# Performance work log

Hardware: AMD Instinct MI355X
Metric: run time of the kernel (lower is better)

The kernel has to match this reference:

```python
import jax, jax.numpy as jnp
import numpy as np


def setup_inputs() -> dict:
    B, L, D, M, S = 4, 1024, 1024, 16, 8
    key = jax.random.key(0)
    ks = jax.random.split(key, 12)
    sd = 0.02
    inp = {
        "hid": jax.random.normal(ks[0], (B, L, D), jnp.float32),
        "src_hid": jax.random.normal(ks[1], (B, L, D), jnp.float32),
        "sp_width": jax.random.randint(ks[2], (B, L), 0, 9),
        "max_sp_len": S,
        "attention_mask": jnp.ones((B, L), bool),
        "src_mask": jnp.ones((B, L), bool),
        # span-start attention (1 head): query/key linears + relative-key embedding table
        "wq_st": sd * jax.random.normal(ks[3], (D, D), jnp.float32),
        "bq_st": jnp.zeros((D,), jnp.float32),
        "wk_st": sd * jax.random.normal(ks[4], (D, D), jnp.float32),
        "bk_st": jnp.zeros((D,), jnp.float32),
        "rel_st": sd * jax.random.normal(ks[5], (2 * M + 1, D), jnp.float32),
        # span-end attention
        "wq_ed": sd * jax.random.normal(ks[6], (D, D), jnp.float32),
        "bq_ed": jnp.zeros((D,), jnp.float32),
        "wk_ed": sd * jax.random.normal(ks[7], (D, D), jnp.float32),
        "bk_ed": jnp.zeros((D,), jnp.float32),
        "rel_ed": sd * jax.random.normal(ks[8], (2 * M + 1, D), jnp.float32),
        # sp_emb: Linear(2D -> D), stored as [2D, D] (x @ W + b)
        "sp_w": sd * jax.random.normal(ks[9], (2 * D, D), jnp.float32),
        "sp_b": jnp.zeros((D,), jnp.float32),
    }
    return inp


def reference(hid, src_hid, sp_width, max_sp_len, attention_mask, src_mask,
              wq_st, bq_st, wk_st, bk_st, rel_st,
              wq_ed, bq_ed, wk_ed, bk_ed, rel_ed, sp_w, sp_b):
    B, L, D = hid.shape
    scale = 1.0 / jnp.sqrt(jnp.float32(D))
    M = (rel_st.shape[0] - 1) // 2
    pos = jnp.arange(L)
    rel_idx = jnp.clip(pos[None, :] - pos[:, None], -M, M) + M          # [L,L]
    rel_idx_b = jnp.broadcast_to(rel_idx[None], (B, L, L))

    amask = (src_mask[:, :, None] & attention_mask[:, None, :]).astype(jnp.float32)  # [B,Lq,Lk]
    attn_w0 = amask / jnp.clip(jnp.sum(amask, 2, keepdims=True), 1e-6)

    def attn(query, wq, bq, wk, bk, rel_tab, mask):
        # single-head relative-position attention; returns attention weights [B,L,L]
        q = (query @ wq + bq) * scale                                   # [B,L,D]
        k = hid @ wk + bk                                               # [B,L,D]
        sc = jnp.einsum('bqd,bkd->bqk', q, k)
        # q . rel_emb[rel_idx[q_pos,k_pos]]: contract with table then gather (avoids [L,L,D])
        rel_sc = jnp.take_along_axis(jnp.einsum('bqd,rd->bqr', q, rel_tab), rel_idx_b, axis=2)
        sc = jnp.where(mask > 0, sc + rel_sc, -1e18)
        return jax.nn.softmax(sc, axis=-1)

    def upd(attn_w, hidp):
        # weighted sum of hid + linear + relu (dropout is identity in eval)
        hidc = jnp.einsum('bqk,bkd->bqd', attn_w, hid)
        return jax.nn.relu(jnp.concatenate([hidp, hidc], axis=2) @ sp_w + sp_b)

    sts, eds, masks = [attn_w0], [attn_w0], []
    hid1, hid2 = src_hid, src_hid
    for i in range(max_sp_len):
        m = (i < sp_width).astype(jnp.float32)                          # [B,L]
        masks.append(m)
        mask_i = m[:, :, None] * amask                                  # [B,L,L]
        hid1 = upd(sts[-1], hid1)
        sts.append(attn(hid1, wq_st, bq_st, wk_st, bk_st, rel_st, mask_i))
        hid2 = upd(eds[-1], hid2)
        eds.append(attn(hid2, wq_ed, bq_ed, wk_ed, bk_ed, rel_ed, mask_i))

    return (jnp.stack(sts[1:], -2),   # [B,L,S,L]
            jnp.stack(eds[1:], -2),   # [B,L,S,L]
            jnp.stack(masks, -1))     # [B,L,S]
```

## Files before the change

kernel.cpp:

```cpp
#include <hip/hip_runtime.h>

typedef unsigned short u16;
typedef __attribute__((ext_vector_type(8))) short bh8;
typedef __attribute__((ext_vector_type(4))) float f4;

__device__ __forceinline__ u16 f2b(float x){
  union { float f; unsigned u; } c; c.f = x;
  unsigned r = (c.u + 0x7FFFu + ((c.u >> 16) & 1u)) >> 16;
  return (u16)r;
}
__device__ __forceinline__ float b2f(u16 h){
  union { unsigned u; float f; } c; c.u = ((unsigned)h) << 16; return c.f;
}
__device__ __forceinline__ void gload16(const void* g, void* l){
  __builtin_amdgcn_global_load_lds((const __attribute__((address_space(1))) void*)g,
                                   (__attribute__((address_space(3))) void*)l, 16, 0, 0);
}


__global__ __launch_bounds__(256) void convall_k(const float* __restrict__ hid,
                                                 const float* __restrict__ wq0, const float* __restrict__ wq1,
                                                 const float* __restrict__ wk0, const float* __restrict__ wk1,
                                                 const float* __restrict__ rel0, const float* __restrict__ rel1,
                                                 u16* __restrict__ hidB, u16* __restrict__ wqB,
                                                 u16* __restrict__ wkB, u16* __restrict__ relB){
  long g = (long)blockIdx.x*256 + threadIdx.x;
  if (g >= 2114048L) return;
  const float* src; u16* dst; long off;
  if      (g < 1048576L){ src = hid;  dst = hidB;           off = g; }
  else if (g < 1310720L){ src = wq0;  dst = wqB;            off = g - 1048576L; }
  else if (g < 1572864L){ src = wq1;  dst = wqB + 1048576;  off = g - 1310720L; }
  else if (g < 1835008L){ src = wk0;  dst = wkB;            off = g - 1572864L; }
  else if (g < 2097152L){ src = wk1;  dst = wkB + 1048576;  off = g - 1835008L; }
  else if (g < 2105600L){ src = rel0; dst = relB;           off = g - 2097152L; }
  else                  { src = rel1; dst = relB + 131072;  off = g - 2105600L; }
  f4 v = *(const f4*)(src + off*4);
  ushort4 pk = make_ushort4(f2b(v[0]), f2b(v[1]), f2b(v[2]), f2b(v[3]));
  *(ushort4*)(dst + off*4) = pk;
}

__global__ __launch_bounds__(256) void uniform0_k(const int* __restrict__ spw, float* __restrict__ out){
  int bl = blockIdx.x;
  if (spw[bl] != 0) return;
  f4 t = {0.0009765625f, 0.0009765625f, 0.0009765625f, 0.0009765625f};
  float* b0 = out + (size_t)bl*8192;
  float* b1 = out + 33554432ull + (size_t)bl*8192;
  #pragma unroll
  for (int i = 0; i < 8; i++){
    ((f4*)(b0 + (size_t)i*1024))[threadIdx.x] = t;
    ((f4*)(b1 + (size_t)i*1024))[threadIdx.x] = t;
  }
}

__global__ __launch_bounds__(256) void trans_k(const float* __restrict__ in, u16* __restrict__ out,
                                               int R, int C){
  __shared__ u16 t[32][33];
  int bx = blockIdx.x*32, by = blockIdx.y*32;
  int tx = threadIdx.x & 31, ty = threadIdx.x >> 5;
  #pragma unroll
  for (int j = 0; j < 32; j += 8) t[ty+j][tx] = f2b(in[(size_t)(by+ty+j)*C + bx+tx]);
  __syncthreads();
  #pragma unroll
  for (int j = 0; j < 32; j += 8) out[(size_t)(bx+ty+j)*R + by+tx] = t[tx][ty+j];
}

__global__ __launch_bounds__(256) void sort_k(const int* __restrict__ spw, int* __restrict__ perm,
                                              int* __restrict__ cnt, float* __restrict__ mout){
  int b = blockIdx.x, t = threadIdx.x;
  __shared__ int hist[9], start[9];
  if (t < 9) hist[t] = 0;
  __syncthreads();
  for (int l = t; l < 1024; l += 256) atomicAdd(&hist[spw[b*1024 + l]], 1);
  __syncthreads();
  if (t == 0){
    int acc = 0;
    for (int w = 8; w >= 0; w--){ start[w] = acc; acc += hist[w]; }
  }
  __syncthreads();
  if (t < 8) cnt[b*8 + t] = start[t];
  __syncthreads();
  for (int l = t; l < 1024; l += 256){
    int w = spw[b*1024 + l];
    float* mo = mout + ((size_t)b*1024 + l)*8;
    #pragma unroll
    for (int i = 0; i < 8; i++) mo[i] = (i < w) ? 1.0f : 0.0f;
    int pos = atomicAdd(&start[w], 1);
    perm[b*1024 + pos] = l;
  }
}

__global__ __launch_bounds__(256) void gather_k(const float* __restrict__ srch, const int* __restrict__ perm,
                                                u16* __restrict__ hb){
  int blk = blockIdx.x;
  int z = blk >> 10, c = blk & 1023;
  int ro = perm[z*1024 + c];
  const float* src = srch + ((size_t)z*1024 + ro)*1024;
  u16* dst = hb + ((size_t)z*1024 + c)*1024;
  for (int d = threadIdx.x; d < 1024; d += 256) dst[d] = f2b(src[d]);
}

__global__ __launch_bounds__(256) void dots_k(const float* __restrict__ wq0, const float* __restrict__ wq1,
                                              const float* __restrict__ wk0, const float* __restrict__ wk1,
                                              const float* __restrict__ bq0, const float* __restrict__ bq1,
                                              const float* __restrict__ bk0, const float* __restrict__ bk1,
                                              const float* __restrict__ rel0, const float* __restrict__ rel1,
                                              float* __restrict__ ubuf, float* __restrict__ c0buf,
                                              float* __restrict__ bqbk, float* __restrict__ cba){
  int row = blockIdx.x*4 + (threadIdx.x >> 6);
  int lane = threadIdx.x & 63;
  if (row >= 4164) return;
  const float *a, *v;
  int kind = 0, oi = 0, br_s = 0, br_r = 0;
  if      (row < 1024){ a = wk0 + (size_t)row*1024; v = bq0; oi = row; }
  else if (row < 2048){ a = wk1 + (size_t)(row-1024)*1024; v = bq1; oi = row; }
  else if (row < 3072){ a = wq0 + (size_t)(row-2048)*1024; v = bk0; kind = 1; oi = row-2048; }
  else if (row < 4096){ a = wq1 + (size_t)(row-3072)*1024; v = bk1; kind = 1; oi = row-3072+1024; }
  else if (row < 4162){ int idx = row-4096; br_s = idx/33; br_r = idx%33;
                        a = (br_s ? rel1 : rel0) + (size_t)br_r*1024; v = br_s ? bq1 : bq0; kind = 2; }
  else                { int s2 = row-4162; a = s2 ? bq1 : bq0; v = s2 ? bk1 : bk0; kind = 3; oi = s2; }
  const f4* ap = (const f4*)a;
  const f4* vp = (const f4*)v;
  float acc = 0.0f;
  #pragma unroll
  for (int p = 0; p < 4; p++){
    f4 x = ap[lane + 64*p], y = vp[lane + 64*p];
    acc += x[0]*y[0] + x[1]*y[1] + x[2]*y[2] + x[3]*y[3];
  }
  #pragma unroll
  for (int off = 32; off > 0; off >>= 1) acc += __shfl_xor(acc, off, 64);
  if (lane == 0){
    if (kind == 0) ubuf[oi] = acc;
    else if (kind == 1) c0buf[oi] = acc;
    else if (kind == 2){
      float w = acc*0.03125f;
      for (int b = 0; b < 4; b++) cba[(br_s*4 + b)*1152 + 1024 + br_r] = w;
    } else bqbk[oi] = acc;
  }
}

__global__ __launch_bounds__(256) void cba_k(const float* __restrict__ hid, const float* __restrict__ u,
                                             const float* __restrict__ bqbk, float* __restrict__ cba){
  int row = blockIdx.x*4 + (threadIdx.x >> 6);
  int lane = threadIdx.x & 63;
  int z = row >> 10, l = row & 1023, b = z & 3, s = z >> 2;
  const f4* hp = (const f4*)(hid + ((size_t)b*1024 + l)*1024);
  const f4* up = (const f4*)(u + s*1024);
  float acc = 0.0f;
  #pragma unroll
  for (int p = 0; p < 4; p++){
    f4 a = hp[lane + 64*p], c = up[lane + 64*p];
    acc += a[0]*c[0] + a[1]*c[1] + a[2]*c[2] + a[3]*c[3];
  }
  #pragma unroll
  for (int off = 32; off > 0; off >>= 1) acc += __shfl_xor(acc, off, 64);
  if (!lane) cba[z*1152 + l] = (acc + bqbk[s])*0.03125f;
}

__global__ __launch_bounds__(256) void meanh2_k(const u16* __restrict__ H2T, float* __restrict__ mh){
  int row = blockIdx.x*4 + (threadIdx.x >> 6);
  int lane = threadIdx.x & 63;
  const u16* p = H2T + (size_t)row*1024 + lane*16;
  float s = 0.0f;
  #pragma unroll
  for (int j = 0; j < 16; j++) s += b2f(p[j]);
  #pragma unroll
  for (int off = 32; off > 0; off >>= 1) s += __shfl_xor(s, off, 64);
  if (lane == 0) mh[row] = s * 0.0009765625f;
}

__global__ __launch_bounds__(256) void softmax_k(const u16* __restrict__ scB, float* __restrict__ outF,
                                                 u16* __restrict__ attnP, const float* __restrict__ qrelb,
                                                 const int* __restrict__ cnt, const int* __restrict__ perm,
                                                 const int* __restrict__ spw, int iter){
  int z = blockIdx.x >> 10, c = blockIdx.x & 1023;
  int s = z >> 2, b = z & 3;
  if (c >= cnt[b*8 + iter]) return;
  int ro = perm[b*1024 + c];
  __shared__ float qr[33];
  __shared__ float red[8];
  if (threadIdx.x < 33) qr[threadIdx.x] = qrelb[((size_t)z*1024 + c)*33 + threadIdx.x];
  __syncthreads();
  const u16* sc = scB + ((size_t)z*1024 + c)*1024;
  float* po = outF + (size_t)s*33554432ull + (((size_t)(b*1024 + ro))*8 + (size_t)iter)*1024;
  u16* pr = attnP + ((size_t)z*1024 + c)*1024;
  int t = threadIdx.x;
  float v[4]; float mx = -1e30f;
  #pragma unroll
  for (int j = 0; j < 4; j++){
    int col = t + j*256;
    int d = col - ro; d = d < -16 ? -16 : (d > 16 ? 16 : d);
    v[j] = b2f(sc[col]) + qr[d + 16];
    mx = fmaxf(mx, v[j]);
  }
  #pragma unroll
  for (int off = 32; off > 0; off >>= 1) mx = fmaxf(mx, __shfl_xor(mx, off, 64));
  int wv = t >> 6, ln = t & 63;
  if (ln == 0) red[wv] = mx;
  __syncthreads();
  mx = fmaxf(fmaxf(red[0], red[1]), fmaxf(red[2], red[3]));
  float sm = 0.0f;
  #pragma unroll
  for (int j = 0; j < 4; j++){ v[j] = __expf(v[j] - mx); sm += v[j]; }
  #pragma unroll
  for (int off = 32; off > 0; off >>= 1) sm += __shfl_xor(sm, off, 64);
  if (ln == 0) red[4 + wv] = sm;
  __syncthreads();
  sm = red[4] + red[5] + red[6] + red[7];
  float inv = 1.0f / sm;
  #pragma unroll
  for (int j = 0; j < 4; j++){
    float pv = v[j] * inv;
    po[t + j*256] = pv;
    pr[t + j*256] = f2b(pv);
  }
  int w = spw[b*1024 + ro];
  if (iter == w - 1 && w < 8){
    f4 u = {0.0009765625f, 0.0009765625f, 0.0009765625f, 0.0009765625f};
    for (int j = 1; j <= 7 - iter; j++)
      ((f4*)(po + (size_t)j*1024))[t] = u;
  }
}

template<int MODE>
__global__ __launch_bounds__(256) void gemm_k(
    const u16* __restrict__ A_, const u16* __restrict__ B_,
    const u16* __restrict__ A2_, const u16* __restrict__ B2_,
    const float* __restrict__ e0, const float* __restrict__ e1,
    u16* __restrict__ outB, u16* __restrict__ outB2, float* __restrict__ qrelb,
    const int* __restrict__ cnt, int iter, int azmask)
{
  const int z = blockIdx.z;
  const size_t LD = 1024*1024;
  const int bm = blockIdx.y*128, bn = blockIdx.x*128;
  int s = z >> 2, b = z & 3;
  bool m5h2 = false;
  if constexpr (MODE == 5){ if (z >= 8){ m5h2 = true; b = z - 8; s = 0; } }

  int cntv = 1024;
  if constexpr (MODE == 2 || MODE == 4){
    cntv = cnt[b*8 + iter];
    if (bm >= cntv) return;
  }

  const u16 *A1, *B1, *A2, *B2;
  int lda1 = 1024, ldb1 = 1024, lda2 = 1024, ldb2 = 1024, K = 1024, K1 = 1024;

  if constexpr (MODE == 0){
    if (z < 2){ A1 = A_ + (size_t)z*LD; B1 = B_ + (size_t)z*LD; }
    else {
      if (blockIdx.y > 0) return;
      A1 = A2_ + (size_t)(z-2)*131072;
      B1 = A_ + (size_t)(z-2)*LD;
    }
    A2=A1; B2=B1;
  }
  else if constexpr (MODE == 2){
    A1 = A_ + (size_t)z*LD; B1 = B_ + (size_t)b*LD;
    A2 = A2_ + (size_t)(z & azmask)*LD; B2 = B2_; ldb2 = 2048;
    if (iter == 0){ K = 1024; K1 = 0; } else { K = 2048; K1 = 1024; }
  }
  else if constexpr (MODE == 4){ A1 = A_ + (size_t)(z & azmask)*LD; B1 = B_ + (size_t)z*1179648; A2=A1; B2=B1; }
  else {
    if (!m5h2){ A1 = A_ + (size_t)b*LD; B1 = B_ + (size_t)s*LD; }
    else      { A1 = A2_ + 1024; lda1 = 2048; B1 = B2_ + (size_t)b*LD; }
    A2=A1; B2=B1; lda2=lda1;
  }

  __shared__ __align__(16) u16 lA[16384];
  __shared__ __align__(16) u16 lB[16384];
  const int tid = threadIdx.x, wv = tid >> 6, lane = tid & 63;
  const int wr = (wv >> 1)*64, wc = (wv & 1)*64;
  const int fr = lane & 15, kh = lane >> 4;
  const int stRow = (lane >> 2);
  const int ssw  = ((lane >> 2) & 3) ^ ((lane >> 4) & 3);
  const int stCe = ((lane & 3) ^ ssw)*8;
  const int fsw  = (fr & 3) ^ ((fr >> 2) & 3);
  const int rdSl = (kh ^ fsw)*8;

  auto stage = [&](int bufsel, int k0s){
    const u16 *As, *Bs; int kk, la, lb;
    if (k0s < K1){ As = A1; Bs = B1; kk = k0s; la = lda1; lb = ldb1; }
    else         { As = A2; Bs = B2; kk = k0s - K1; la = lda2; lb = ldb2; }
    #pragma unroll
    for (int c = 0; c < 4; c++){
      const int n = wv*4 + c;
      const int h = n >> 3;
      const int rl = (n & 7)*16 + stRow;
      const int ke = kk + h*32 + stCe;
      gload16(As + (size_t)(bm + rl)*la + ke, (char*)lA + bufsel*16384 + n*1024);
      gload16(Bs + (size_t)(bn + rl)*lb + ke, (char*)lB + bufsel*16384 + n*1024);
    }
  };

  f4 acc[4][4];
  #pragma unroll
  for (int i = 0; i < 4; i++)
    #pragma unroll
    for (int j = 0; j < 4; j++)
      acc[i][j] = f4{0.f, 0.f, 0.f, 0.f};

  stage(0, 0);
  stage(1, 64);

  int cur = 0;
  for (int k0 = 0; k0 < K; k0 += 64){
    if (k0 + 64 < K) asm volatile("s_waitcnt vmcnt(8)" ::: "memory");
    else             asm volatile("s_waitcnt vmcnt(0)" ::: "memory");
    __builtin_amdgcn_s_barrier();
    asm volatile("" ::: "memory");
    const u16* bufA = lA + cur*8192;
    const u16* bufB = lB + cur*8192;
    bh8 af[2][4], bfr[2][4];
    #pragma unroll
    for (int h = 0; h < 2; h++){
      #pragma unroll
      for (int i = 0; i < 4; i++){
        af[h][i]  = *(const bh8*)&bufA[h*4096 + (wr + i*16 + fr)*32 + rdSl];
        bfr[h][i] = *(const bh8*)&bufB[h*4096 + (wc + i*16 + fr)*32 + rdSl];
      }
    }
    if (k0 + 128 < K){
      asm volatile("s_waitcnt lgkmcnt(0)" ::: "memory");
      __builtin_amdgcn_sched_barrier(0);
      __builtin_amdgcn_s_barrier();
      asm volatile("" ::: "memory");
      stage(cur, k0 + 128);
    }
    __builtin_amdgcn_s_setprio(1);
    #pragma unroll
    for (int h = 0; h < 2; h++)
      #pragma unroll
      for (int i = 0; i < 4; i++)
        #pragma unroll
        for (int j = 0; j < 4; j++)
          acc[i][j] = __builtin_amdgcn_mfma_f32_16x16x32_bf16(af[h][i], bfr[h][j], acc[i][j], 0, 0, 0);
    __builtin_amdgcn_s_setprio(0);
    cur ^= 1;
  }

  const int rw = (lane >> 4)*4, cl = lane & 15;
  #pragma unroll
  for (int i = 0; i < 4; i++){
    #pragma unroll
    for (int r = 0; r < 4; r++){
      const int row = bm + wr + i*16 + rw + r;
      if constexpr (MODE == 2 || MODE == 4){ if (row >= cntv) continue; }
      #pragma unroll
      for (int j = 0; j < 4; j++){
        const int col = bn + wc + j*16 + cl;
        float v = acc[i][j][r];
        if constexpr (MODE == 0){
          if (z < 2){
            outB[(size_t)z*LD + (size_t)row*1024 + col] = f2b(v);
          } else if (row < 33){
            u16 vv = f2b(v*0.03125f);
            size_t o = (size_t)(1024 + row)*1024 + col;
            int sx = z - 2;
            #pragma unroll
            for (int bb = 0; bb < 4; bb++)
              outB2[(size_t)(sx*4 + bb)*1179648 + o] = vv;
          }
        } else if constexpr (MODE == 2){
          v += e0[col];
          if (e1) v += e1[b*1024 + col];
          v = fmaxf(v, 0.0f);
          outB[(size_t)z*LD + (size_t)row*1024 + col] = f2b(v);
        } else if constexpr (MODE == 5){
          if (!m5h2)
            outB[(size_t)z*1179648 + (size_t)row*1024 + col] = f2b((v + e0[s*1024 + col])*0.03125f);
          else
            outB2[(size_t)b*LD + (size_t)row*1024 + col] = f2b(v);
        } else {
          v += e0[z*1152 + col];
          if (col < 1024){
            outB[((size_t)z*1024 + row)*1024 + col] = f2b(v);
          } else {
            int rr = col - 1024;
            if (rr < 33) qrelb[((size_t)z*1024 + row)*33 + rr] = v;
          }
        }
      }
    }
  }
}


extern "C" void kernel_launch(void* const* d_in, const int* in_sizes, int n_in,
                              void* d_out, int out_size, void* d_ws, size_t ws_size,
                              hipStream_t stream)
{
  const float* hid    = (const float*)d_in[0];
  const float* srch   = (const float*)d_in[1];
  const int*   spw    = (const int*)d_in[2];
  const float* wq_st  = (const float*)d_in[6];
  const float* bq_st  = (const float*)d_in[7];
  const float* wk_st  = (const float*)d_in[8];
  const float* bk_st  = (const float*)d_in[9];
  const float* rel_st = (const float*)d_in[10];
  const float* wq_ed  = (const float*)d_in[11];
  const float* bq_ed  = (const float*)d_in[12];
  const float* wk_ed  = (const float*)d_in[13];
  const float* bk_ed  = (const float*)d_in[14];
  const float* rel_ed = (const float*)d_in[15];
  const float* sp_w   = (const float*)d_in[16];
  const float* sp_b   = (const float*)d_in[17];
  float* out = (float*)d_out;

  const size_t LD = 1024*1024;
  char* p = (char*)d_ws;
  u16* hidB  = (u16*)p; p += 4*LD*2;
  u16* wqB   = (u16*)p; p += 2*LD*2;
  u16* wkB   = (u16*)p; p += 2*LD*2;
  u16* relB  = (u16*)p; p += 2*131072*2;
  u16* spwT  = (u16*)p; p += 2*LD*2;
  u16* WT    = (u16*)p; p += 2*LD*2;
  u16* H2T   = (u16*)p; p += 4*LD*2;
  u16* Mx    = (u16*)p; p += 8ull*1179648*2;
  u16* attnP = (u16*)p; p += 8*LD*2;
  u16* hbufA = (u16*)p; p += 8*LD*2;
  u16* hbufB = (u16*)p; p += 8*LD*2;
  u16* scB   = (u16*)p; p += 8*LD*2;
  float* qrelb  = (float*)p; p += 8*1024*33*4;
  float* cba    = (float*)p; p += 8*1152*4;
  float* ubuf   = (float*)p; p += 2048*4;
  float* c0buf  = (float*)p; p += 2048*4;
  float* bqbk   = (float*)p; p += 64;
  float* meanH2 = (float*)p; p += 4*1024*4;
  int*   perm   = (int*)p;   p += 4*1024*4;
  int*   cnt    = (int*)p;   p += 1024;

  const dim3 t256(256);

  convall_k<<<8258, t256, 0, stream>>>(hid, wq_st, wq_ed, wk_st, wk_ed, rel_st, rel_ed,
                                       hidB, wqB, wkB, relB);
  sort_k<<<4, t256, 0, stream>>>(spw, perm, cnt, out + 67108864ull);
  gather_k<<<4096, t256, 0, stream>>>(srch, perm, hbufA);
  uniform0_k<<<4096, t256, 0, stream>>>(spw, out);
  trans_k<<<dim3(32,64), t256, 0, stream>>>(sp_w, spwT, 2048, 1024);
  dots_k<<<1041, t256, 0, stream>>>(wq_st, wq_ed, wk_st, wk_ed, bq_st, bq_ed, bk_st, bk_ed,
                                    rel_st, rel_ed, ubuf, c0buf, bqbk, cba);
  cba_k<<<2048, t256, 0, stream>>>(hid, ubuf, bqbk, cba);

  gemm_k<0><<<dim3(8,8,4), t256, 0, stream>>>(wqB, wkB, relB, nullptr, nullptr, nullptr,
                                              WT, Mx, nullptr, nullptr, 0, 7);
  gemm_k<5><<<dim3(8,8,12), t256, 0, stream>>>(hidB, WT, spwT, hidB, c0buf, nullptr,
                                               Mx, H2T, nullptr, nullptr, 0, 7);
  meanh2_k<<<1024, t256, 0, stream>>>(H2T, meanH2);

  u16* hp = hbufA; u16* hn = hbufB;
  for (int i = 0; i < 8; i++){
    int g2z = (i == 0) ? 4 : 8;
    int am2 = (i <= 1) ? 3 : 7;
    gemm_k<2><<<dim3(8,8,g2z), t256, 0, stream>>>(attnP, H2T, hp, spwT, sp_b,
                                                  (i == 0) ? meanH2 : nullptr,
                                                  hn, nullptr, nullptr, cnt, i, am2);
    int am4 = (i == 0) ? 3 : 7;
    gemm_k<4><<<dim3(9,8,8), t256, 0, stream>>>(hn, Mx, nullptr, nullptr, cba, nullptr,
                                                scB, nullptr, qrelb, cnt, i, am4);
    softmax_k<<<8192, t256, 0, stream>>>(scB, out, attnP, qrelb, cnt, perm, spw, i);
    u16* tmp = hp; hp = hn; hn = tmp;
  }
}
```

Baseline: 820.7 us.

## Merge setup kernels into two fused launches and compute meanH2 from mean hid

Folds the separate conversion, gather, uniform-fill, transpose and dot-product setup kernels into one multi-role kernel, and merges the cba kernel with a new meanH2 computation into a second. meanH2 is now computed algebraically as the column-mean of hid projected through the transposed sp_w half, rather than by averaging the H2T rows after the gemm. This cuts launch count and removes the dependence of meanH2 on the gemm_k<5> output. The column-mean loop is serial over 1024 rows in only 16 blocks, which may be slow. Numerics change slightly because meanH2 no longer averages bf16-rounded H2T.

```diff
diff --git a/kernel.cpp b/kernel.cpp
--- a/kernel.cpp
+++ b/kernel.cpp
@@ -15,53 +15,6 @@
 __device__ __forceinline__ void gload16(const void* g, void* l){
   __builtin_amdgcn_global_load_lds((const __attribute__((address_space(1))) void*)g,
                                    (__attribute__((address_space(3))) void*)l, 16, 0, 0);
-}
-
-
-__global__ __launch_bounds__(256) void convall_k(const float* __restrict__ hid,
-                                                 const float* __restrict__ wq0, const float* __restrict__ wq1,
-                                                 const float* __restrict__ wk0, const float* __restrict__ wk1,
-                                                 const float* __restrict__ rel0, const float* __restrict__ rel1,
-                                                 u16* __restrict__ hidB, u16* __restrict__ wqB,
-                                                 u16* __restrict__ wkB, u16* __restrict__ relB){
-  long g = (long)blockIdx.x*256 + threadIdx.x;
-  if (g >= 2114048L) return;
-  const float* src; u16* dst; long off;
-  if      (g < 1048576L){ src = hid;  dst = hidB;           off = g; }
-  else if (g < 1310720L){ src = wq0;  dst = wqB;            off = g - 1048576L; }
-  else if (g < 1572864L){ src = wq1;  dst = wqB + 1048576;  off = g - 1310720L; }
-  else if (g < 1835008L){ src = wk0;  dst = wkB;            off = g - 1572864L; }
-  else if (g < 2097152L){ src = wk1;  dst = wkB + 1048576;  off = g - 1835008L; }
-  else if (g < 2105600L){ src = rel0; dst = relB;           off = g - 2097152L; }
-  else                  { src = rel1; dst = relB + 131072;  off = g - 2105600L; }
-  f4 v = *(const f4*)(src + off*4);
-  ushort4 pk = make_ushort4(f2b(v[0]), f2b(v[1]), f2b(v[2]), f2b(v[3]));
-  *(ushort4*)(dst + off*4) = pk;
-}
-
-__global__ __launch_bounds__(256) void uniform0_k(const int* __restrict__ spw, float* __restrict__ out){
-  int bl = blockIdx.x;
-  if (spw[bl] != 0) return;
-  f4 t = {0.0009765625f, 0.0009765625f, 0.0009765625f, 0.0009765625f};
-  float* b0 = out + (size_t)bl*8192;
-  float* b1 = out + 33554432ull + (size_t)bl*8192;
-  #pragma unroll
-  for (int i = 0; i < 8; i++){
-    ((f4*)(b0 + (size_t)i*1024))[threadIdx.x] = t;
-    ((f4*)(b1 + (size_t)i*1024))[threadIdx.x] = t;
-  }
-}
-
-__global__ __launch_bounds__(256) void trans_k(const float* __restrict__ in, u16* __restrict__ out,
-                                               int R, int C){
-  __shared__ u16 t[32][33];
-  int bx = blockIdx.x*32, by = blockIdx.y*32;
-  int tx = threadIdx.x & 31, ty = threadIdx.x >> 5;
-  #pragma unroll
-  for (int j = 0; j < 32; j += 8) t[ty+j][tx] = f2b(in[(size_t)(by+ty+j)*C + bx+tx]);
-  __syncthreads();
-  #pragma unroll
-  for (int j = 0; j < 32; j += 8) out[(size_t)(bx+ty+j)*R + by+tx] = t[tx][ty+j];
 }
 
 __global__ __launch_bounds__(256) void sort_k(const int* __restrict__ spw, int* __restrict__ perm,
@@ -89,83 +42,144 @@
   }
 }
 
-__global__ __launch_bounds__(256) void gather_k(const float* __restrict__ srch, const int* __restrict__ perm,
-                                                u16* __restrict__ hb){
-  int blk = blockIdx.x;
-  int z = blk >> 10, c = blk & 1023;
-  int ro = perm[z*1024 + c];
-  const float* src = srch + ((size_t)z*1024 + ro)*1024;
-  u16* dst = hb + ((size_t)z*1024 + c)*1024;
-  for (int d = threadIdx.x; d < 1024; d += 256) dst[d] = f2b(src[d]);
-}
-
-__global__ __launch_bounds__(256) void dots_k(const float* __restrict__ wq0, const float* __restrict__ wq1,
-                                              const float* __restrict__ wk0, const float* __restrict__ wk1,
-                                              const float* __restrict__ bq0, const float* __restrict__ bq1,
-                                              const float* __restrict__ bk0, const float* __restrict__ bk1,
-                                              const float* __restrict__ rel0, const float* __restrict__ rel1,
-                                              float* __restrict__ ubuf, float* __restrict__ c0buf,
-                                              float* __restrict__ bqbk, float* __restrict__ cba){
-  int row = blockIdx.x*4 + (threadIdx.x >> 6);
-  int lane = threadIdx.x & 63;
-  if (row >= 4164) return;
-  const float *a, *v;
-  int kind = 0, oi = 0, br_s = 0, br_r = 0;
-  if      (row < 1024){ a = wk0 + (size_t)row*1024; v = bq0; oi = row; }
-  else if (row < 2048){ a = wk1 + (size_t)(row-1024)*1024; v = bq1; oi = row; }
-  else if (row < 3072){ a = wq0 + (size_t)(row-2048)*1024; v = bk0; kind = 1; oi = row-2048; }
-  else if (row < 4096){ a = wq1 + (size_t)(row-3072)*1024; v = bk1; kind = 1; oi = row-3072+1024; }
-  else if (row < 4162){ int idx = row-4096; br_s = idx/33; br_r = idx%33;
-                        a = (br_s ? rel1 : rel0) + (size_t)br_r*1024; v = br_s ? bq1 : bq0; kind = 2; }
-  else                { int s2 = row-4162; a = s2 ? bq1 : bq0; v = s2 ? bk1 : bk0; kind = 3; oi = s2; }
-  const f4* ap = (const f4*)a;
-  const f4* vp = (const f4*)v;
-  float acc = 0.0f;
-  #pragma unroll
-  for (int p = 0; p < 4; p++){
-    f4 x = ap[lane + 64*p], y = vp[lane + 64*p];
-    acc += x[0]*y[0] + x[1]*y[1] + x[2]*y[2] + x[3]*y[3];
-  }
-  #pragma unroll
-  for (int off = 32; off > 0; off >>= 1) acc += __shfl_xor(acc, off, 64);
-  if (lane == 0){
-    if (kind == 0) ubuf[oi] = acc;
-    else if (kind == 1) c0buf[oi] = acc;
-    else if (kind == 2){
-      float w = acc*0.03125f;
-      for (int b = 0; b < 4; b++) cba[(br_s*4 + b)*1152 + 1024 + br_r] = w;
-    } else bqbk[oi] = acc;
-  }
-}
-
-__global__ __launch_bounds__(256) void cba_k(const float* __restrict__ hid, const float* __restrict__ u,
-                                             const float* __restrict__ bqbk, float* __restrict__ cba){
-  int row = blockIdx.x*4 + (threadIdx.x >> 6);
-  int lane = threadIdx.x & 63;
-  int z = row >> 10, l = row & 1023, b = z & 3, s = z >> 2;
-  const f4* hp = (const f4*)(hid + ((size_t)b*1024 + l)*1024);
-  const f4* up = (const f4*)(u + s*1024);
-  float acc = 0.0f;
-  #pragma unroll
-  for (int p = 0; p < 4; p++){
-    f4 a = hp[lane + 64*p], c = up[lane + 64*p];
-    acc += a[0]*c[0] + a[1]*c[1] + a[2]*c[2] + a[3]*c[3];
-  }
-  #pragma unroll
-  for (int off = 32; off > 0; off >>= 1) acc += __shfl_xor(acc, off, 64);
-  if (!lane) cba[z*1152 + l] = (acc + bqbk[s])*0.03125f;
-}
-
-__global__ __launch_bounds__(256) void meanh2_k(const u16* __restrict__ H2T, float* __restrict__ mh){
-  int row = blockIdx.x*4 + (threadIdx.x >> 6);
-  int lane = threadIdx.x & 63;
-  const u16* p = H2T + (size_t)row*1024 + lane*16;
-  float s = 0.0f;
-  #pragma unroll
-  for (int j = 0; j < 16; j++) s += b2f(p[j]);
-  #pragma unroll
-  for (int off = 32; off > 0; off >>= 1) s += __shfl_xor(s, off, 64);
-  if (lane == 0) mh[row] = s * 0.0009765625f;
+__global__ __launch_bounds__(256) void mega1_k(const float* __restrict__ hid,
+                                               const float* __restrict__ srch,
+                                               const int* __restrict__ spw,
+                                               const int* __restrict__ perm,
+                                               const float* __restrict__ wq0, const float* __restrict__ wq1,
+                                               const float* __restrict__ wk0, const float* __restrict__ wk1,
+                                               const float* __restrict__ bq0, const float* __restrict__ bq1,
+                                               const float* __restrict__ bk0, const float* __restrict__ bk1,
+                                               const float* __restrict__ rel0, const float* __restrict__ rel1,
+                                               const float* __restrict__ sp_w,
+                                               u16* __restrict__ hidB, u16* __restrict__ wqB,
+                                               u16* __restrict__ wkB, u16* __restrict__ relB,
+                                               u16* __restrict__ hb, float* __restrict__ outF,
+                                               u16* __restrict__ spwT,
+                                               float* __restrict__ ubuf, float* __restrict__ c0buf,
+                                               float* __restrict__ bqbk, float* __restrict__ cba,
+                                               float* __restrict__ mean_hid){
+  __shared__ u16 tt[32][33];
+  const int blk = blockIdx.x, tid = threadIdx.x;
+  if (blk < 8258){
+    long g = (long)blk*256 + tid;
+    if (g >= 2114048L) return;
+    const float* src; u16* dst; long off;
+    if      (g < 1048576L){ src = hid;  dst = hidB;           off = g; }
+    else if (g < 1310720L){ src = wq0;  dst = wqB;            off = g - 1048576L; }
+    else if (g < 1572864L){ src = wq1;  dst = wqB + 1048576;  off = g - 1310720L; }
+    else if (g < 1835008L){ src = wk0;  dst = wkB;            off = g - 1572864L; }
+    else if (g < 2097152L){ src = wk1;  dst = wkB + 1048576;  off = g - 1835008L; }
+    else if (g < 2105600L){ src = rel0; dst = relB;           off = g - 2097152L; }
+    else                  { src = rel1; dst = relB + 131072;  off = g - 2105600L; }
+    f4 v = *(const f4*)(src + off*4);
+    ushort4 pk = make_ushort4(f2b(v[0]), f2b(v[1]), f2b(v[2]), f2b(v[3]));
+    *(ushort4*)(dst + off*4) = pk;
+  } else if (blk < 12354){
+    int b2 = blk - 8258;
+    int z = b2 >> 10, c = b2 & 1023;
+    int ro = perm[z*1024 + c];
+    const float* src = srch + ((size_t)z*1024 + ro)*1024;
+    u16* dst = hb + ((size_t)z*1024 + c)*1024;
+    for (int d = tid; d < 1024; d += 256) dst[d] = f2b(src[d]);
+  } else if (blk < 16450){
+    int bl = blk - 12354;
+    if (spw[bl] != 0) return;
+    f4 t = {0.0009765625f, 0.0009765625f, 0.0009765625f, 0.0009765625f};
+    float* b0 = outF + (size_t)bl*8192;
+    float* b1 = outF + 33554432ull + (size_t)bl*8192;
+    #pragma unroll
+    for (int i = 0; i < 8; i++){
+      ((f4*)(b0 + (size_t)i*1024))[tid] = t;
+      ((f4*)(b1 + (size_t)i*1024))[tid] = t;
+    }
+  } else if (blk < 18498){
+    int t2 = blk - 16450;
+    int bx = (t2 & 31)*32, by = (t2 >> 5)*32;
+    int tx = tid & 31, ty = tid >> 5;
+    #pragma unroll
+    for (int j = 0; j < 32; j += 8) tt[ty+j][tx] = f2b(sp_w[(size_t)(by+ty+j)*1024 + bx+tx]);
+    __syncthreads();
+    #pragma unroll
+    for (int j = 0; j < 32; j += 8) spwT[(size_t)(bx+ty+j)*2048 + by+tx] = tt[tx][ty+j];
+  } else if (blk < 19539){
+    int row = (blk - 18498)*4 + (tid >> 6);
+    int lane = tid & 63;
+    if (row >= 4164) return;
+    const float *a, *v;
+    int kind = 0, oi = 0, br_s = 0, br_r = 0;
+    if      (row < 1024){ a = wk0 + (size_t)row*1024; v = bq0; oi = row; }
+    else if (row < 2048){ a = wk1 + (size_t)(row-1024)*1024; v = bq1; oi = row; }
+    else if (row < 3072){ a = wq0 + (size_t)(row-2048)*1024; v = bk0; kind = 1; oi = row-2048; }
+    else if (row < 4096){ a = wq1 + (size_t)(row-3072)*1024; v = bk1; kind = 1; oi = row-3072+1024; }
+    else if (row < 4162){ int idx = row-4096; br_s = idx/33; br_r = idx%33;
+                          a = (br_s ? rel1 : rel0) + (size_t)br_r*1024; v = br_s ? bq1 : bq0; kind = 2; }
+    else                { int s2 = row-4162; a = s2 ? bq1 : bq0; v = s2 ? bk1 : bk0; kind = 3; oi = s2; }
+    const f4* ap = (const f4*)a;
+    const f4* vp = (const f4*)v;
+    float acc = 0.0f;
+    #pragma unroll
+    for (int p = 0; p < 4; p++){
+      f4 x = ap[lane + 64*p], y = vp[lane + 64*p];
+      acc += x[0]*y[0] + x[1]*y[1] + x[2]*y[2] + x[3]*y[3];
+    }
+    #pragma unroll
+    for (int off = 32; off > 0; off >>= 1) acc += __shfl_xor(acc, off, 64);
+    if (lane == 0){
+      if (kind == 0) ubuf[oi] = acc;
+      else if (kind == 1) c0buf[oi] = acc;
+      else if (kind == 2){
+        float w = acc*0.03125f;
+        for (int b = 0; b < 4; b++) cba[(br_s*4 + b)*1152 + 1024 + br_r] = w;
+      } else bqbk[oi] = acc;
+    }
+  } else {
+    int t2 = blk - 19539;
+    if (t2 >= 16) return;
+    int b = t2 >> 2, ch = t2 & 3;
+    int k = ch*256 + tid;
+    const float* base = hid + (size_t)b*1048576 + k;
+    float acc = 0.0f;
+    for (int l = 0; l < 1024; l++) acc += base[(size_t)l*1024];
+    mean_hid[b*1024 + k] = acc * 0.0009765625f;
+  }
+}
+
+__global__ __launch_bounds__(256) void mega2_k(const float* __restrict__ hid, const float* __restrict__ u,
+                                               const float* __restrict__ bqbk, float* __restrict__ cba,
+                                               const u16* __restrict__ spwT, const float* __restrict__ mean_hid,
+                                               float* __restrict__ meanH2){
+  int blk = blockIdx.x, tid = threadIdx.x;
+  int lane = tid & 63;
+  if (blk < 2048){
+    int row = blk*4 + (tid >> 6);
+    int z = row >> 10, l = row & 1023, b = z & 3, s = z >> 2;
+    const f4* hp = (const f4*)(hid + ((size_t)b*1024 + l)*1024);
+    const f4* up = (const f4*)(u + s*1024);
+    float acc = 0.0f;
+    #pragma unroll
+    for (int p = 0; p < 4; p++){
+      f4 a = hp[lane + 64*p], c = up[lane + 64*p];
+      acc += a[0]*c[0] + a[1]*c[1] + a[2]*c[2] + a[3]*c[3];
+    }
+    #pragma unroll
+    for (int off = 32; off > 0; off >>= 1) acc += __shfl_xor(acc, off, 64);
+    if (!lane) cba[z*1152 + l] = (acc + bqbk[s])*0.03125f;
+  } else {
+    int row = (blk - 2048)*4 + (tid >> 6);
+    int b = row >> 10, d = row & 1023;
+    const u16* wrow = spwT + (size_t)d*2048 + 1024;
+    const float* mh = mean_hid + b*1024;
+    float acc = 0.0f;
+    #pragma unroll
+    for (int p = 0; p < 16; p++){
+      int k = lane + 64*p;
+      acc += b2f(wrow[k]) * mh[k];
+    }
+    #pragma unroll
+    for (int off = 32; off > 0; off >>= 1) acc += __shfl_xor(acc, off, 64);
+    if (!lane) meanH2[row] = acc;
+  }
 }
 
 __global__ __launch_bounds__(256) void softmax_k(const u16* __restrict__ scB, float* __restrict__ outF,
@@ -426,26 +440,24 @@
   float* c0buf  = (float*)p; p += 2048*4;
   float* bqbk   = (float*)p; p += 64;
   float* meanH2 = (float*)p; p += 4*1024*4;
+  float* mean_hid = (float*)p; p += 4*1024*4;
   int*   perm   = (int*)p;   p += 4*1024*4;
   int*   cnt    = (int*)p;   p += 1024;
 
   const dim3 t256(256);
 
-  convall_k<<<8258, t256, 0, stream>>>(hid, wq_st, wq_ed, wk_st, wk_ed, rel_st, rel_ed,
-                                       hidB, wqB, wkB, relB);
   sort_k<<<4, t256, 0, stream>>>(spw, perm, cnt, out + 67108864ull);
-  gather_k<<<4096, t256, 0, stream>>>(srch, perm, hbufA);
-  uniform0_k<<<4096, t256, 0, stream>>>(spw, out);
-  trans_k<<<dim3(32,64), t256, 0, stream>>>(sp_w, spwT, 2048, 1024);
-  dots_k<<<1041, t256, 0, stream>>>(wq_st, wq_ed, wk_st, wk_ed, bq_st, bq_ed, bk_st, bk_ed,
-                                    rel_st, rel_ed, ubuf, c0buf, bqbk, cba);
-  cba_k<<<2048, t256, 0, stream>>>(hid, ubuf, bqbk, cba);
+  mega1_k<<<19555, t256, 0, stream>>>(hid, srch, spw, perm,
+                                      wq_st, wq_ed, wk_st, wk_ed, bq_st, bq_ed, bk_st, bk_ed,
+                                      rel_st, rel_ed, sp_w,
+                                      hidB, wqB, wkB, relB, hbufA, out, spwT,
+                                      ubuf, c0buf, bqbk, cba, mean_hid);
+  mega2_k<<<3072, t256, 0, stream>>>(hid, ubuf, bqbk, cba, spwT, mean_hid, meanH2);
 
   gemm_k<0><<<dim3(8,8,4), t256, 0, stream>>>(wqB, wkB, relB, nullptr, nullptr, nullptr,
                                               WT, Mx, nullptr, nullptr, 0, 7);
   gemm_k<5><<<dim3(8,8,12), t256, 0, stream>>>(hidB, WT, spwT, hidB, c0buf, nullptr,
                                                Mx, H2T, nullptr, nullptr, 0, 7);
-  meanh2_k<<<1024, t256, 0, stream>>>(H2T, meanH2);
 
   u16* hp = hbufA; u16* hn = hbufB;
   for (int i = 0; i < 8; i++){
```

Measured after the change: 849.9 us. 3.6% more time.
